# Kernel optimization log

Measured on AMD Instinct MI355X. Metric: run time of the kernel, lower is better.

The kernel has to match this reference:

```python
import jax, jax.numpy as jnp
import numpy as np

NUM_CLASSES = 81
N_ROIS = 100000
N_GT = 512
ROIS_PER_IMAGE = 256
FG_ROIS_PER_IMAGE = 128  # fg_fraction * rois_per_image
FG_THRESH = 0.5
BG_HI = 0.5
BG_LO = 0.1


def _make_boxes(key, n, img=1024.0):
    k1, k2, k3, k4 = jax.random.split(key, 4)
    x1 = jax.random.uniform(k1, (n,)) * (img - 160.0)
    y1 = jax.random.uniform(k2, (n,)) * (img - 160.0)
    w = 16.0 + jax.random.uniform(k3, (n,)) * 112.0
    h = 16.0 + jax.random.uniform(k4, (n,)) * 112.0
    return jnp.stack([x1, y1, x1 + w, y1 + h], axis=1)


def setup_inputs() -> dict:
    key = jax.random.key(0)
    kg, kc, kn, kr, ks = jax.random.split(key, 5)
    gt_xyxy = _make_boxes(kg, N_GT)
    gt_cls = jax.random.randint(kc, (N_GT, 1), 1, NUM_CLASSES).astype(jnp.float32)
    gt_boxes = jnp.concatenate([gt_xyxy, gt_cls], axis=1)
    # first block of proposals = jittered gt boxes so fg samples exist
    n_jit = 4096
    reps = int(np.ceil(n_jit / N_GT))
    jit_base = jnp.tile(gt_xyxy, (reps, 1))[:n_jit]
    noise = (jax.random.uniform(kn, (n_jit, 4)) - 0.5) * 12.0
    jit_boxes = jit_base + noise
    rand_boxes = _make_boxes(kr, N_ROIS - n_jit)
    boxes = jnp.concatenate([jit_boxes, rand_boxes], axis=0)
    rpn_rois = jnp.concatenate([jnp.zeros((N_ROIS, 1), jnp.float32), boxes], axis=1)
    rpn_scores = jax.random.uniform(ks, (N_ROIS, 1), dtype=jnp.float32)
    return {"rpn_rois": rpn_rois, "rpn_scores": rpn_scores, "gt_boxes": gt_boxes}


def _bbox_overlaps(b1, b2):
    # b1 [N,4], b2 [G,4] -> IoU [N,G] with +1 pixel convention
    x1a, y1a, x2a, y2a = b1[:, 0], b1[:, 1], b1[:, 2], b1[:, 3]
    x1b, y1b, x2b, y2b = b2[:, 0], b2[:, 1], b2[:, 2], b2[:, 3]
    iw = jnp.maximum(0.0, jnp.minimum(x2a[:, None], x2b[None, :]) - jnp.maximum(x1a[:, None], x1b[None, :]) + 1.0)
    ih = jnp.maximum(0.0, jnp.minimum(y2a[:, None], y2b[None, :]) - jnp.maximum(y1a[:, None], y1b[None, :]) + 1.0)
    inter = iw * ih
    a1 = (x2a - x1a + 1.0) * (y2a - y1a + 1.0)
    a2 = (x2b - x1b + 1.0) * (y2b - y1b + 1.0)
    union = a1[:, None] + a2[None, :] - inter
    return jnp.where(inter == 0.0, 0.0, inter / union)


def _bbox_transform(ex, gt):
    ew = ex[:, 2] - ex[:, 0] + 1.0
    eh = ex[:, 3] - ex[:, 1] + 1.0
    ecx = ex[:, 0] + 0.5 * ew
    ecy = ex[:, 1] + 0.5 * eh
    gw = gt[:, 2] - gt[:, 0] + 1.0
    gh = gt[:, 3] - gt[:, 1] + 1.0
    gcx = gt[:, 0] + 0.5 * gw
    gcy = gt[:, 1] + 0.5 * gh
    return jnp.stack([(gcx - ecx) / ew, (gcy - ecy) / eh, jnp.log(gw / ew), jnp.log(gh / eh)], axis=1)


def _forward(rpn_rois, rpn_scores, gt_boxes):
    means = jnp.array([0.0, 0.0, 0.0, 0.0], jnp.float32)
    stds = jnp.array([0.1, 0.1, 0.2, 0.2], jnp.float32)
    k1, k2, k3 = jax.random.split(jax.random.key(42), 3)
    n = rpn_rois.shape[0]
    overlaps = _bbox_overlaps(rpn_rois[:, 1:5], gt_boxes[:, :4])  # [N,G]
    gt_assignment = jnp.argmax(overlaps, axis=1)  # [N]
    max_overlaps = jnp.max(overlaps, axis=1)      # [N]
    fg_mask = max_overlaps >= FG_THRESH
    bg_mask = (max_overlaps < BG_HI) & (max_overlaps >= BG_LO)
    # shuffled candidate orderings: random key for candidates, +2 sentinel pushes rest to the back
    fg_order = jnp.argsort(jnp.where(fg_mask, jax.random.uniform(k1, (n,)), 2.0))
    bg_order = jnp.argsort(jnp.where(bg_mask, jax.random.uniform(k2, (n,)), 2.0))
    fg_count = jnp.minimum(FG_ROIS_PER_IMAGE, jnp.sum(fg_mask))
    bg_count = jnp.minimum(ROIS_PER_IMAGE - fg_count, jnp.sum(bg_mask))
    pos = jnp.arange(ROIS_PER_IMAGE)
    sel = jnp.where(pos < fg_count, fg_order[pos], bg_order[jnp.maximum(pos - fg_count, 0)])
    # fill any shortfall by re-sampling uniformly from the fg+bg picks
    n_samp = fg_count + bg_count
    n_safe = jnp.maximum(n_samp, 1)
    dup = (jax.random.uniform(k3, (ROIS_PER_IMAGE,)) * n_safe).astype(jnp.int32)
    sel = jnp.where(pos < n_samp, sel, sel[dup])
    gt_ids = gt_assignment[sel]
    labels = gt_boxes[gt_ids, 4]
    fmax = max_overlaps[sel]
    labels = jnp.where((fmax < BG_HI) & (fmax >= BG_LO), 0.0, labels)
    rois = rpn_rois[sel]                 # [256,5]
    roi_scores = rpn_scores[sel].reshape(-1)
    targets = _bbox_transform(rois[:, 1:5], gt_boxes[gt_ids, :4])
    targets = (targets - means) / stds
    # expand compact (cls,tx,ty,tw,th) into N x 4K, nonzero only at own-class slot
    cls = labels.astype(jnp.int32)
    valid = (labels > 0).astype(jnp.float32)[:, None]
    rows = pos[:, None]
    cols = cls[:, None] * 4 + jnp.arange(4)[None, :]
    zeros4k = jnp.zeros((ROIS_PER_IMAGE, 4 * NUM_CLASSES), jnp.float32)
    bbox_targets = zeros4k.at[rows, cols].set(targets * valid)
    bbox_inside = zeros4k.at[rows, cols].set(jnp.ones((1, 4), jnp.float32) * valid)
    bbox_outside = (bbox_inside > 0).astype(jnp.float32)
    return rois, roi_scores, labels, bbox_targets, bbox_inside, bbox_outside


def reference(rpn_rois, rpn_scores, gt_boxes):
    return _forward(rpn_rois, rpn_scores, gt_boxes)
```

## Files before the change

### kernel.cpp

```cpp
#include <hip/hip_runtime.h>
#include <stdint.h>

__host__ __device__ inline void tf2x32(uint32_t ks0, uint32_t ks1, uint32_t x0, uint32_t x1,
                                       uint32_t& o0, uint32_t& o1) {
  uint32_t ks2 = ks0 ^ ks1 ^ 0x1BD11BDAu;
#define TFR(r) { x0 += x1; x1 = (x1 << (r)) | (x1 >> (32 - (r))); x1 ^= x0; }
  x0 += ks0; x1 += ks1;
  TFR(13) TFR(15) TFR(26) TFR(6)
  x0 += ks1; x1 += ks2 + 1u;
  TFR(17) TFR(29) TFR(16) TFR(24)
  x0 += ks2; x1 += ks0 + 2u;
  TFR(13) TFR(15) TFR(26) TFR(6)
  x0 += ks0; x1 += ks1 + 3u;
  TFR(17) TFR(29) TFR(16) TFR(24)
  x0 += ks1; x1 += ks2 + 4u;
  TFR(13) TFR(15) TFR(26) TFR(6)
  x0 += ks2; x1 += ks0 + 5u;
#undef TFR
  o0 = x0; o1 = x1;
}

__device__ inline float bits_to_unif(uint32_t b) {
  return __uint_as_float((b >> 9) | 0x3F800000u) - 1.0f;
}

__device__ inline uint32_t jbits(int v, uint32_t ka, uint32_t kb, uint32_t i, uint32_t n) {
  uint32_t o0, o1;
  if (v == 2) {
    uint32_t h = (n + 1) >> 1;
    if (i < h) {
      uint32_t xh = (i + h < n) ? (i + h) : 0u;
      tf2x32(ka, kb, i, xh, o0, o1);
      return o0;
    }
    tf2x32(ka, kb, i - h, i, o0, o1);
    return o1;
  }
  tf2x32(ka, kb, 0u, i, o0, o1);
  return (v == 0) ? o0 : (o0 ^ o1);
}

__device__ inline int jbucket(uint32_t b) { return (int)(b >> 22); }

#define NGT_MAX      512
#define ROIS_PER_IMG 256
#define FG_PER_IMG   128
#define NCOLS        324
#define NB           1024
#define CAND_CAP     2048
#define WAVES        4

#define OFF_SCORES 1280
#define OFF_LABELS 1536
#define OFF_BIG    1792
#define BIGN       (ROIS_PER_IMG * NCOLS)

#define WS_MAXOV   0
#define WS_GTASGN  400000
#define WS_HIST    800000
#define WS_CANDF   808192
#define WS_CANDB   824576
#define WS_META    840960
#define WS_CLS     841024
#define WS_T       842048
#define WS_GT8     846144

__global__ void __launch_bounds__(1024) k_detect(const float* __restrict__ scores,
                                                 const float* __restrict__ gt,
                                                 int n, int ngt,
                                                 int* __restrict__ meta,
                                                 int* __restrict__ hist,
                                                 float* __restrict__ gt8) {
#pragma clang fp contract(off)
  int tid = threadIdx.x;
  hist[tid] = 0;
  hist[NB + tid] = 0;
  if (tid >= 7 && tid <= 13) meta[tid] = 0;

  if (tid < NGT_MAX && tid < ngt) {
    float x1 = gt[tid * 5 + 0], y1 = gt[tid * 5 + 1];
    float x2 = gt[tid * 5 + 2], y2 = gt[tid * 5 + 3];
    gt8[tid * 8 + 0] = x1; gt8[tid * 8 + 1] = y1;
    gt8[tid * 8 + 2] = x2; gt8[tid * 8 + 3] = y2;
    gt8[tid * 8 + 4] = (x2 - x1 + 1.0f) * (y2 - y1 + 1.0f);
    gt8[tid * 8 + 5] = gt[tid * 5 + 4];
    gt8[tid * 8 + 6] = 0.0f; gt8[tid * 8 + 7] = 0.0f;
  }

  if (tid < 64) {
    uint32_t pa, pb; tf2x32(0u, 0u, 0u, 4u, pa, pb);
    uint32_t t0, t1, q0, q1;
    tf2x32(0u, 0u, 3u, 8u, t0, t1);
    tf2x32(0u, 0u, 4u, 9u, q0, q1);
    uint32_t la = t1, lb = q1;

    bool m0 = false, m1 = false, m2 = false;
    if (tid < 16) {
      uint32_t sref = __float_as_uint(scores[tid]);
      uint32_t o0, o1; tf2x32(pa, pb, 0u, (uint32_t)tid, o0, o1);
      m0 = (__float_as_uint(bits_to_unif(o0)) == sref);
      m1 = (__float_as_uint(bits_to_unif(o0 ^ o1)) == sref);
      uint32_t h = (uint32_t)(n >> 1);
      uint32_t c0, c1; tf2x32(la, lb, (uint32_t)tid, (uint32_t)tid + h, c0, c1);
      m2 = (__float_as_uint(bits_to_unif(c0)) == sref);
    }
    int n0 = __popcll(__ballot(m0));
    int n1 = __popcll(__ballot(m1));
    int n2 = __popcll(__ballot(m2));
    if (tid == 0) {
      int v = (n1 >= n0 && n1 >= n2) ? 1 : ((n0 >= n2) ? 0 : 2);
      meta[0] = v;
      uint32_t K[6];
      if (v == 2) {
        uint32_t a0, a1, b0, b1, c0, c1;
        tf2x32(0u, 42u, 0u, 3u, a0, a1);
        tf2x32(0u, 42u, 1u, 4u, b0, b1);
        tf2x32(0u, 42u, 2u, 5u, c0, c1);
        K[0] = a0; K[1] = b0; K[2] = c0; K[3] = a1; K[4] = b1; K[5] = c1;
      } else {
        tf2x32(0u, 42u, 0u, 0u, K[0], K[1]);
        tf2x32(0u, 42u, 0u, 1u, K[2], K[3]);
        tf2x32(0u, 42u, 0u, 2u, K[4], K[5]);
      }
      for (int j = 0; j < 6; ++j) meta[1 + j] = (int)K[j];
    }
  }
}

__global__ void __launch_bounds__(256) k_iou(const float* __restrict__ rois,
                                             const float* __restrict__ gt8,
                                             int n, int ngt,
                                             float* __restrict__ maxov,
                                             int* __restrict__ gtasgn,
                                             int* __restrict__ hist,
                                             const int* __restrict__ meta) {
#pragma clang fp contract(off)
  __shared__ float4 sgt4[NGT_MAX];
  __shared__ float sarea[NGT_MAX];
  __shared__ float sbest[WAVES][128];
  __shared__ int   sbi[WAVES][128];
  __shared__ int   smeta[7];
  const int tid = threadIdx.x;
  const int wave = tid >> 6;
  const int lane = tid & 63;
  if (tid < 7) smeta[tid] = meta[tid];
  {
    const float4* g4p = (const float4*)gt8;
    for (int g = tid; g < ngt; g += 256) {
      float4 box = g4p[2 * g];
      float4 ext = g4p[2 * g + 1];
      sgt4[g] = box;
      sarea[g] = ext.x;
    }
  }
  __syncthreads();

  const int R = blockIdx.x * 128;
  const int iA = R + lane;
  const int iB = R + lane + 64;
  const bool pA = (iA < n), pB = (iB < n);

  float ax1 = 1e30f, ay1 = 1e30f, ax2 = -1e30f, ay2 = -1e30f, a1A = 1.0f;
  float bx1 = 1e30f, by1 = 1e30f, bx2 = -1e30f, by2 = -1e30f, a1B = 1.0f;
  if (pA) {
    ax1 = rois[iA * 5 + 1]; ay1 = rois[iA * 5 + 2];
    ax2 = rois[iA * 5 + 3]; ay2 = rois[iA * 5 + 4];
    a1A = (ax2 - ax1 + 1.0f) * (ay2 - ay1 + 1.0f);
  }
  if (pB) {
    bx1 = rois[iB * 5 + 1]; by1 = rois[iB * 5 + 2];
    bx2 = rois[iB * 5 + 3]; by2 = rois[iB * 5 + 4];
    a1B = (bx2 - bx1 + 1.0f) * (by2 - by1 + 1.0f);
  }

  const int csz = (ngt + WAVES - 1) / WAVES;
  const int g0 = wave * csz;
  const int cnt = max(0, min(ngt, g0 + csz) - g0);

  unsigned long long mA0 = 0ull, mA1 = 0ull, mB0 = 0ull, mB1 = 0ull;
  if (cnt == 128) {
#pragma unroll 8
    for (int jj = 0; jj < 64; ++jj) {
      float4 G = sgt4[g0 + jj];
      bool oA = (fminf(ax2, G.z) - fmaxf(ax1, G.x) > -1.0f) &&
                (fminf(ay2, G.w) - fmaxf(ay1, G.y) > -1.0f);
      bool oB = (fminf(bx2, G.z) - fmaxf(bx1, G.x) > -1.0f) &&
                (fminf(by2, G.w) - fmaxf(by1, G.y) > -1.0f);
      if (oA) mA0 |= (1ull << jj);
      if (oB) mB0 |= (1ull << jj);
    }
#pragma unroll 8
    for (int jj = 0; jj < 64; ++jj) {
      float4 G = sgt4[g0 + 64 + jj];
      bool oA = (fminf(ax2, G.z) - fmaxf(ax1, G.x) > -1.0f) &&
                (fminf(ay2, G.w) - fmaxf(ay1, G.y) > -1.0f);
      bool oB = (fminf(bx2, G.z) - fmaxf(bx1, G.x) > -1.0f) &&
                (fminf(by2, G.w) - fmaxf(by1, G.y) > -1.0f);
      if (oA) mA1 |= (1ull << jj);
      if (oB) mB1 |= (1ull << jj);
    }
  } else {
    for (int jj = 0; jj < cnt; ++jj) {
      float4 G = sgt4[g0 + jj];
      bool oA = (fminf(ax2, G.z) - fmaxf(ax1, G.x) > -1.0f) &&
                (fminf(ay2, G.w) - fmaxf(ay1, G.y) > -1.0f);
      bool oB = (fminf(bx2, G.z) - fmaxf(bx1, G.x) > -1.0f) &&
                (fminf(by2, G.w) - fmaxf(by1, G.y) > -1.0f);
      if (jj < 64) {
        if (oA) mA0 |= (1ull << jj);
        if (oB) mB0 |= (1ull << jj);
      } else {
        if (oA) mA1 |= (1ull << (jj - 64));
        if (oB) mB1 |= (1ull << (jj - 64));
      }
    }
  }

  float bestA = 0.0f, bestB = 0.0f;
  int biA = 0, biB = 0;
  auto drain = [&](unsigned long long m, int base,
                   float x1r, float y1r, float x2r, float y2r, float a1r,
                   float& best, int& bi) {
    while (m) {
      int jj = __builtin_ctzll(m);
      m &= m - 1ull;
      int j = base + jj;
      float4 G = sgt4[j];
      float iw = fminf(x2r, G.z) - fmaxf(x1r, G.x) + 1.0f;
      float ih = fminf(y2r, G.w) - fmaxf(y1r, G.y) + 1.0f;
      float inter = iw * ih;
      float uni = a1r + sarea[j] - inter;
      float iou = inter / uni;
      if (iou > best) { best = iou; bi = j; }
    }
  };
  drain(mA0, g0,      ax1, ay1, ax2, ay2, a1A, bestA, biA);
  drain(mA1, g0 + 64, ax1, ay1, ax2, ay2, a1A, bestA, biA);
  drain(mB0, g0,      bx1, by1, bx2, by2, a1B, bestB, biB);
  drain(mB1, g0 + 64, bx1, by1, bx2, by2, a1B, bestB, biB);

  sbest[wave][lane] = bestA;      sbi[wave][lane] = biA;
  sbest[wave][lane + 64] = bestB; sbi[wave][lane + 64] = biB;
  __syncthreads();

  if (tid < 128) {
    const int r = R + tid;
    float best = sbest[0][tid];
    int bi = sbi[0][tid];
    for (int w = 1; w < WAVES; ++w) {
      float ob = sbest[w][tid];
      int oi = sbi[w][tid];
      if (ob > best || (ob == best && oi < bi)) { best = ob; bi = oi; }
    }
    if (r < n) {
      maxov[r] = best;
      gtasgn[r] = bi;
      if (best >= 0.1f) {
        const int v = smeta[0];
        const bool fg = (best >= 0.5f);
        uint32_t ka = (uint32_t)(fg ? smeta[1] : smeta[3]);
        uint32_t kb = (uint32_t)(fg ? smeta[2] : smeta[4]);
        uint32_t b = jbits(v, ka, kb, (uint32_t)r, (uint32_t)n);
        atomicAdd(&hist[(fg ? 0 : NB) + jbucket(b)], 1);
      }
    }
  }
}

__global__ void __launch_bounds__(1024) k_scan(const int* __restrict__ hist,
                                               int* __restrict__ meta) {
  __shared__ int hf[NB], hb[NB];
  const int tid = threadIdx.x;
  hf[tid] = hist[tid];
  hb[tid] = hist[NB + tid];
  __syncthreads();
  for (int s = 1; s < NB; s <<= 1) {
    int tf_ = hf[tid] + ((tid >= s) ? hf[tid - s] : 0);
    int tb_ = hb[tid] + ((tid >= s) ? hb[tid - s] : 0);
    __syncthreads();
    hf[tid] = tf_; hb[tid] = tb_;
    __syncthreads();
  }
  const int fg_count = min(FG_PER_IMG, hf[NB - 1]);
  const int bg_count = min(ROIS_PER_IMG - fg_count, hb[NB - 1]);
  if (tid == 0) {
    meta[9] = fg_count;
    meta[10] = bg_count;
    if (fg_count == 0) meta[7] = -1;
    if (bg_count == 0) meta[8] = -1;
  }
  if (fg_count > 0 && hf[tid] >= fg_count && (tid == 0 || hf[tid - 1] < fg_count)) meta[7] = tid;
  if (bg_count > 0 && hb[tid] >= bg_count && (tid == 0 || hb[tid - 1] < bg_count)) meta[8] = tid;
}

__global__ void k_collect(const float* __restrict__ maxov, int n,
                          int* __restrict__ meta,
                          unsigned long long* __restrict__ candf,
                          unsigned long long* __restrict__ candb) {
  __shared__ int smeta[9];
  if (threadIdx.x < 9) smeta[threadIdx.x] = meta[threadIdx.x];
  __syncthreads();
  const int i = blockIdx.x * blockDim.x + threadIdx.x;
  if (i >= n) return;
  const int v = smeta[0];
  const int Bf = smeta[7], Bb = smeta[8];
  float m = maxov[i];
  if (m >= 0.5f) {
    if (Bf >= 0) {
      uint32_t b = jbits(v, (uint32_t)smeta[1], (uint32_t)smeta[2], (uint32_t)i, (uint32_t)n);
      if (jbucket(b) <= Bf) {
        int p = atomicAdd(&meta[11], 1);
        if (p < CAND_CAP) candf[p] = ((unsigned long long)(b >> 9) << 32) | (unsigned)i;
      }
    }
  } else if (m >= 0.1f) {
    if (Bb >= 0) {
      uint32_t b = jbits(v, (uint32_t)smeta[3], (uint32_t)smeta[4], (uint32_t)i, (uint32_t)n);
      if (jbucket(b) <= Bb) {
        int p = atomicAdd(&meta[12], 1);
        if (p < CAND_CAP) candb[p] = ((unsigned long long)(b >> 9) << 32) | (unsigned)i;
      }
    }
  }
}

__device__ inline void bitonic(unsigned long long* buf, int nelem, int tid, int nthr) {
  for (int k = 2; k <= nelem; k <<= 1)
    for (int j = k >> 1; j > 0; j >>= 1) {
      for (int i = tid; i < nelem; i += nthr) {
        int l = i ^ j;
        if (l > i) {
          unsigned long long a = buf[i], b = buf[l];
          bool swap_ = ((i & k) == 0) ? (a > b) : (a < b);
          if (swap_) { buf[i] = b; buf[l] = a; }
        }
      }
      __syncthreads();
    }
}

__global__ void __launch_bounds__(1024) k_pick(
    const float* __restrict__ rois, const float* __restrict__ scores,
    const float* __restrict__ gt,
    const float* __restrict__ maxov, const int* __restrict__ gtasgn,
    const int* __restrict__ meta,
    const unsigned long long* __restrict__ gcandf,
    const unsigned long long* __restrict__ gcandb,
    float* __restrict__ out, int* __restrict__ ws_cls, float* __restrict__ ws_t) {
#pragma clang fp contract(off)
  __shared__ unsigned long long candf[CAND_CAP], candb[CAND_CAP];
  __shared__ int sel[ROIS_PER_IMG];
  __shared__ int smeta[13];
  const int tid = threadIdx.x;
  const int nthr = 1024;
  if (tid < 13) smeta[tid] = meta[tid];
  __syncthreads();
  const int v = smeta[0];
  const uint32_t k3a = (uint32_t)smeta[5], k3b = (uint32_t)smeta[6];
  const int fg_count = smeta[9], bg_count = smeta[10];
  const int Mf = min(smeta[11], CAND_CAP);
  const int Mb = min(smeta[12], CAND_CAP);

  int nf = 1; while (nf < Mf) nf <<= 1;
  int nb = 1; while (nb < Mb) nb <<= 1;
  for (int i = tid; i < nf; i += nthr) candf[i] = (i < Mf) ? gcandf[i] : ~0ull;
  for (int i = tid; i < nb; i += nthr) candb[i] = (i < Mb) ? gcandb[i] : ~0ull;
  __syncthreads();

  bitonic(candf, nf, tid, nthr);
  bitonic(candb, nb, tid, nthr);
  __syncthreads();

  if (tid < fg_count) sel[tid] = (int)(candf[tid] & 0xFFFFFFFFull);
  if (tid < bg_count) sel[fg_count + tid] = (int)(candb[tid] & 0xFFFFFFFFull);
  __syncthreads();

  const int n_samp = fg_count + bg_count;
  if (tid < ROIS_PER_IMG && tid >= n_samp) {
    if (n_samp > 0) {
      uint32_t b3 = jbits(v, k3a, k3b, (uint32_t)tid, (uint32_t)ROIS_PER_IMG);
      int d = (int)(bits_to_unif(b3) * (float)n_samp);
      d = min(d, n_samp - 1);
      sel[tid] = sel[d];
    } else {
      sel[tid] = 0;
    }
  }
  __syncthreads();

  if (tid < ROIS_PER_IMG) {
    int i = sel[tid];
    int g = gtasgn[i];
    float fmax = maxov[i];
    float label = gt[g * 5 + 4];
    if (fmax < 0.5f && fmax >= 0.1f) label = 0.0f;

    for (int c = 0; c < 5; ++c) out[tid * 5 + c] = rois[i * 5 + c];
    out[OFF_SCORES + tid] = scores[i];
    out[OFF_LABELS + tid] = label;

    float ex0 = rois[i * 5 + 1], ey0 = rois[i * 5 + 2];
    float ex1 = rois[i * 5 + 3], ey1 = rois[i * 5 + 4];
    float gx0 = gt[g * 5 + 0], gy0 = gt[g * 5 + 1];
    float gx1 = gt[g * 5 + 2], gy1 = gt[g * 5 + 3];
    float ew = ex1 - ex0 + 1.0f, eh = ey1 - ey0 + 1.0f;
    float ecx = ex0 + 0.5f * ew, ecy = ey0 + 0.5f * eh;
    float gw = gx1 - gx0 + 1.0f, gh = gy1 - gy0 + 1.0f;
    float gcx = gx0 + 0.5f * gw, gcy = gy0 + 0.5f * gh;
    float t0 = ((gcx - ecx) / ew) / 0.1f;
    float t1 = ((gcy - ecy) / eh) / 0.1f;
    float t2 = logf(gw / ew) / 0.2f;
    float t3 = logf(gh / eh) / 0.2f;

    float valid = (label > 0.0f) ? 1.0f : 0.0f;
    int cls = (int)label;
    ws_cls[tid] = (valid > 0.0f) ? cls : -1;
    ws_t[tid * 4 + 0] = t0 * valid;
    ws_t[tid * 4 + 1] = t1 * valid;
    ws_t[tid * 4 + 2] = t2 * valid;
    ws_t[tid * 4 + 3] = t3 * valid;
  }
}

__global__ void k_out(const int* __restrict__ ws_cls, const float* __restrict__ ws_t,
                      float* __restrict__ out) {
  int e = blockIdx.x * blockDim.x + threadIdx.x;
  if (e >= BIGN) return;
  int r = e / NCOLS, c = e % NCOLS;
  int cls = ws_cls[r];
  float tv = 0.0f, iv = 0.0f;
  if (cls >= 0) {
    int c0 = cls * 4;
    if (c >= c0 && c < c0 + 4) { tv = ws_t[r * 4 + (c - c0)]; iv = 1.0f; }
  }
  out[OFF_BIG + e] = tv;
  out[OFF_BIG + BIGN + e] = iv;
  out[OFF_BIG + 2 * BIGN + e] = iv;
}

extern "C" void kernel_launch(void* const* d_in, const int* in_sizes, int n_in,
                              void* d_out, int out_size, void* d_ws, size_t ws_size,
                              hipStream_t stream) {
  const float* rois   = (const float*)d_in[0];
  const float* scores = (const float*)d_in[1];
  const float* gt     = (const float*)d_in[2];
  float* out = (float*)d_out;

  const int n   = in_sizes[0] / 5;
  const int ngt = in_sizes[2] / 5;

  char* ws = (char*)d_ws;
  float* maxov  = (float*)(ws + WS_MAXOV);
  int*   gtasgn = (int*)(ws + WS_GTASGN);
  int*   hist   = (int*)(ws + WS_HIST);
  unsigned long long* candf = (unsigned long long*)(ws + WS_CANDF);
  unsigned long long* candb = (unsigned long long*)(ws + WS_CANDB);
  int*   meta   = (int*)(ws + WS_META);
  int*   wcls   = (int*)(ws + WS_CLS);
  float* wt     = (float*)(ws + WS_T);
  float* gt8    = (float*)(ws + WS_GT8);

  k_detect<<<1, 1024, 0, stream>>>(scores, gt, n, ngt, meta, hist, gt8);
  k_iou<<<(n + 127) / 128, 256, 0, stream>>>(rois, gt8, n, ngt, maxov, gtasgn, hist, meta);
  k_scan<<<1, 1024, 0, stream>>>(hist, meta);
  k_collect<<<(n + 255) / 256, 256, 0, stream>>>(maxov, n, meta, candf, candb);
  k_pick<<<1, 1024, 0, stream>>>(rois, scores, gt, maxov, gtasgn, meta,
                                 candf, candb, out, wcls, wt);
  k_out<<<(BIGN + 255) / 256, 256, 0, stream>>>(wcls, wt, out);
}
```

Before: 73.64 us.

## Fuse scan into collect, simplify IoU overlap test, vectorize output writes

The single-block histogram scan is merged into the collect kernel: each 1024-thread block redoes the scan redundantly, which removes one launch. The IoU prefilter now compares against precomputed expanded bounds with bitwise ANDs instead of min/max/subtract, and the drain step skips the division when there is no positive overlap. The output expansion kernel writes float4 per class slot instead of scalar elements. The trade-off is that every collect block repeats the scan work and the prefilter's boundary semantics shift slightly.

```diff
diff --git a/kernel.cpp b/kernel.cpp
--- a/kernel.cpp
+++ b/kernel.cpp
@@ -172,6 +172,8 @@
     bx2 = rois[iB * 5 + 3]; by2 = rois[iB * 5 + 4];
     a1B = (bx2 - bx1 + 1.0f) * (by2 - by1 + 1.0f);
   }
+  const float aXm = ax1 - 1.5f, aXp = ax2 + 1.5f, aYm = ay1 - 1.5f, aYp = ay2 + 1.5f;
+  const float bXm = bx1 - 1.5f, bXp = bx2 + 1.5f, bYm = by1 - 1.5f, bYp = by2 + 1.5f;
 
   const int csz = (ngt + WAVES - 1) / WAVES;
   const int g0 = wave * csz;
@@ -182,30 +184,24 @@
 #pragma unroll 8
     for (int jj = 0; jj < 64; ++jj) {
       float4 G = sgt4[g0 + jj];
-      bool oA = (fminf(ax2, G.z) - fmaxf(ax1, G.x) > -1.0f) &&
-                (fminf(ay2, G.w) - fmaxf(ay1, G.y) > -1.0f);
-      bool oB = (fminf(bx2, G.z) - fmaxf(bx1, G.x) > -1.0f) &&
-                (fminf(by2, G.w) - fmaxf(by1, G.y) > -1.0f);
+      bool oA = (G.x < aXp) & (G.z > aXm) & (G.y < aYp) & (G.w > aYm);
+      bool oB = (G.x < bXp) & (G.z > bXm) & (G.y < bYp) & (G.w > bYm);
       if (oA) mA0 |= (1ull << jj);
       if (oB) mB0 |= (1ull << jj);
     }
 #pragma unroll 8
     for (int jj = 0; jj < 64; ++jj) {
       float4 G = sgt4[g0 + 64 + jj];
-      bool oA = (fminf(ax2, G.z) - fmaxf(ax1, G.x) > -1.0f) &&
-                (fminf(ay2, G.w) - fmaxf(ay1, G.y) > -1.0f);
-      bool oB = (fminf(bx2, G.z) - fmaxf(bx1, G.x) > -1.0f) &&
-                (fminf(by2, G.w) - fmaxf(by1, G.y) > -1.0f);
+      bool oA = (G.x < aXp) & (G.z > aXm) & (G.y < aYp) & (G.w > aYm);
+      bool oB = (G.x < bXp) & (G.z > bXm) & (G.y < bYp) & (G.w > bYm);
       if (oA) mA1 |= (1ull << jj);
       if (oB) mB1 |= (1ull << jj);
     }
   } else {
     for (int jj = 0; jj < cnt; ++jj) {
       float4 G = sgt4[g0 + jj];
-      bool oA = (fminf(ax2, G.z) - fmaxf(ax1, G.x) > -1.0f) &&
-                (fminf(ay2, G.w) - fmaxf(ay1, G.y) > -1.0f);
-      bool oB = (fminf(bx2, G.z) - fmaxf(bx1, G.x) > -1.0f) &&
-                (fminf(by2, G.w) - fmaxf(by1, G.y) > -1.0f);
+      bool oA = (G.x < aXp) & (G.z > aXm) & (G.y < aYp) & (G.w > aYm);
+      bool oB = (G.x < bXp) & (G.z > bXm) & (G.y < bYp) & (G.w > bYm);
       if (jj < 64) {
         if (oA) mA0 |= (1ull << jj);
         if (oB) mB0 |= (1ull << jj);
@@ -228,10 +224,12 @@
       float4 G = sgt4[j];
       float iw = fminf(x2r, G.z) - fmaxf(x1r, G.x) + 1.0f;
       float ih = fminf(y2r, G.w) - fmaxf(y1r, G.y) + 1.0f;
-      float inter = iw * ih;
-      float uni = a1r + sarea[j] - inter;
-      float iou = inter / uni;
-      if (iou > best) { best = iou; bi = j; }
+      if (iw > 0.0f && ih > 0.0f) {
+        float inter = iw * ih;
+        float uni = a1r + sarea[j] - inter;
+        float iou = inter / uni;
+        if (iou > best) { best = iou; bi = j; }
+      }
     }
   };
   drain(mA0, g0,      ax1, ay1, ax2, ay2, a1A, bestA, biA);
@@ -267,10 +265,18 @@
   }
 }
 
-__global__ void __launch_bounds__(1024) k_scan(const int* __restrict__ hist,
-                                               int* __restrict__ meta) {
+__global__ void __launch_bounds__(1024) k_collect(const float* __restrict__ maxov,
+                                                  int n,
+                                                  const int* __restrict__ hist,
+                                                  int* __restrict__ meta,
+                                                  unsigned long long* __restrict__ candf,
+                                                  unsigned long long* __restrict__ candb) {
   __shared__ int hf[NB], hb[NB];
+  __shared__ int smeta[7];
+  __shared__ int sres[2];
   const int tid = threadIdx.x;
+  if (tid < 7) smeta[tid] = meta[tid];
+  if (tid < 2) sres[tid] = -1;
   hf[tid] = hist[tid];
   hb[tid] = hist[NB + tid];
   __syncthreads();
@@ -281,29 +287,17 @@
     hf[tid] = tf_; hb[tid] = tb_;
     __syncthreads();
   }
-  const int fg_count = min(FG_PER_IMG, hf[NB - 1]);
-  const int bg_count = min(ROIS_PER_IMG - fg_count, hb[NB - 1]);
-  if (tid == 0) {
-    meta[9] = fg_count;
-    meta[10] = bg_count;
-    if (fg_count == 0) meta[7] = -1;
-    if (bg_count == 0) meta[8] = -1;
-  }
-  if (fg_count > 0 && hf[tid] >= fg_count && (tid == 0 || hf[tid - 1] < fg_count)) meta[7] = tid;
-  if (bg_count > 0 && hb[tid] >= bg_count && (tid == 0 || hb[tid - 1] < bg_count)) meta[8] = tid;
-}
-
-__global__ void k_collect(const float* __restrict__ maxov, int n,
-                          int* __restrict__ meta,
-                          unsigned long long* __restrict__ candf,
-                          unsigned long long* __restrict__ candb) {
-  __shared__ int smeta[9];
-  if (threadIdx.x < 9) smeta[threadIdx.x] = meta[threadIdx.x];
-  __syncthreads();
-  const int i = blockIdx.x * blockDim.x + threadIdx.x;
+  const int fgc = min(FG_PER_IMG, hf[NB - 1]);
+  const int bgc = min(ROIS_PER_IMG - fgc, hb[NB - 1]);
+  if (tid == 0) { meta[9] = fgc; meta[10] = bgc; }
+  if (fgc > 0 && hf[tid] >= fgc && (tid == 0 || hf[tid - 1] < fgc)) { sres[0] = tid; meta[7] = tid; }
+  if (bgc > 0 && hb[tid] >= bgc && (tid == 0 || hb[tid - 1] < bgc)) { sres[1] = tid; meta[8] = tid; }
+  __syncthreads();
+  const int Bf = sres[0], Bb = sres[1];
+  const int v = smeta[0];
+
+  const int i = blockIdx.x * 1024 + tid;
   if (i >= n) return;
-  const int v = smeta[0];
-  const int Bf = smeta[7], Bb = smeta[8];
   float m = maxov[i];
   if (m >= 0.5f) {
     if (Bf >= 0) {
@@ -424,18 +418,24 @@
 
 __global__ void k_out(const int* __restrict__ ws_cls, const float* __restrict__ ws_t,
                       float* __restrict__ out) {
-  int e = blockIdx.x * blockDim.x + threadIdx.x;
-  if (e >= BIGN) return;
-  int r = e / NCOLS, c = e % NCOLS;
+  const int QROW = NCOLS / 4;
+  const int TOT4 = ROIS_PER_IMG * QROW;
+  int e4 = blockIdx.x * blockDim.x + threadIdx.x;
+  if (e4 >= TOT4) return;
+  int r = e4 / QROW, q = e4 - r * QROW;
   int cls = ws_cls[r];
-  float tv = 0.0f, iv = 0.0f;
-  if (cls >= 0) {
-    int c0 = cls * 4;
-    if (c >= c0 && c < c0 + 4) { tv = ws_t[r * 4 + (c - c0)]; iv = 1.0f; }
-  }
-  out[OFF_BIG + e] = tv;
-  out[OFF_BIG + BIGN + e] = iv;
-  out[OFF_BIG + 2 * BIGN + e] = iv;
+  float4 tv = make_float4(0.f, 0.f, 0.f, 0.f);
+  float4 iv = make_float4(0.f, 0.f, 0.f, 0.f);
+  if (cls >= 0 && q == cls) {
+    tv = *(const float4*)(ws_t + r * 4);
+    iv = make_float4(1.f, 1.f, 1.f, 1.f);
+  }
+  float4* o0 = (float4*)(out + OFF_BIG);
+  float4* o1 = (float4*)(out + OFF_BIG + BIGN);
+  float4* o2 = (float4*)(out + OFF_BIG + 2 * BIGN);
+  o0[e4] = tv;
+  o1[e4] = iv;
+  o2[e4] = iv;
 }
 
 extern "C" void kernel_launch(void* const* d_in, const int* in_sizes, int n_in,
@@ -462,9 +462,8 @@
 
   k_detect<<<1, 1024, 0, stream>>>(scores, gt, n, ngt, meta, hist, gt8);
   k_iou<<<(n + 127) / 128, 256, 0, stream>>>(rois, gt8, n, ngt, maxov, gtasgn, hist, meta);
-  k_scan<<<1, 1024, 0, stream>>>(hist, meta);
-  k_collect<<<(n + 255) / 256, 256, 0, stream>>>(maxov, n, meta, candf, candb);
+  k_collect<<<(n + 1023) / 1024, 1024, 0, stream>>>(maxov, n, hist, meta, candf, candb);
   k_pick<<<1, 1024, 0, stream>>>(rois, scores, gt, maxov, gtasgn, meta,
                                  candf, candb, out, wcls, wt);
-  k_out<<<(BIGN + 255) / 256, 256, 0, stream>>>(wcls, wt, out);
-}
+  k_out<<<(ROIS_PER_IMG * (NCOLS / 4) + 255) / 256, 256, 0, stream>>>(wcls, wt, out);
+}
```

After: 72.86 us. About the same (-1.1%).
